# Kernel optimization log

Hardware: AMD Instinct MI355X
Metric: run time of the kernel (lower is better)

Reference implementation:

```python
import jax, jax.numpy as jnp
import numpy as np

BETA = 0.25
NUM_CODEBOOK = 1024
DIM = 256


def setup_inputs() -> dict:
    key = jax.random.key(0)
    k1, k2 = jax.random.split(key)
    z = jax.random.normal(k1, (32, DIM, 32, 32), dtype=jnp.float32)
    # nn.init.uniform_(weight, -1/num_codebook, 1/num_codebook)
    bound = 1.0 / NUM_CODEBOOK
    codebook = jax.random.uniform(k2, (NUM_CODEBOOK, DIM), dtype=jnp.float32,
                                  minval=-bound, maxval=bound)
    return {"z": z, "codebook": codebook}


def reference(z, codebook):
    B, C, H, W = z.shape
    # NCHW -> NHWC -> [B*H*W, C]
    z_flat = jnp.transpose(z, (0, 2, 3, 1)).reshape(-1, C)
    # squared euclidean distances to each code: [B*H*W, K]
    dist = (jnp.sum(z_flat * z_flat, axis=1, keepdims=True)
            + jnp.sum(codebook * codebook, axis=1)
            - 2.0 * jnp.matmul(z_flat, codebook.T))
    idx = jnp.argmin(dist, axis=-1)                      # [B*H*W]
    z_q = codebook[idx].reshape(B, H, W, C)              # gather
    z_q = jnp.transpose(z_q, (0, 3, 1, 2))               # back to NCHW
    commit_loss = (jnp.mean((jax.lax.stop_gradient(z_q) - z) ** 2)
                   + BETA * jnp.mean((z_q - jax.lax.stop_gradient(z)) ** 2))
    # straight-through estimator
    z_q_st = z + jax.lax.stop_gradient(z_q - z)
    return z_q_st, commit_loss
```

## Files before the change

### kernel.cpp

```cpp
#include <hip/hip_runtime.h>
#include <hip/hip_bf16.h>
#include <hip/hip_fp8.h>
#include <stdint.h>


#define WS_CN    0
#define WS_CB    4096
#define WS_PENC  266240
#define WS_PART2 790528
#define WS_PART  791040

typedef float f32x4 __attribute__((ext_vector_type(4)));
typedef long  i64;
typedef long  l64x2 __attribute__((ext_vector_type(2)));

template <bool HI>
static __device__ __forceinline__ unsigned pk2(float a, float b, unsigned old) {
#if __has_builtin(__builtin_amdgcn_cvt_pk_fp8_f32)
    return (unsigned)__builtin_amdgcn_cvt_pk_fp8_f32(a, b, (int)old, HI);
#else
    __hip_fp8_e4m3 qa(a), qb(b);
    unsigned w = (unsigned)qa.__x | ((unsigned)qb.__x << 8);
    return HI ? ((old & 0x0000FFFFu) | (w << 16)) : ((old & 0xFFFF0000u) | w);
#endif
}

__global__ __launch_bounds__(64) void k0_prep(const float* __restrict__ cb,
                                              float* __restrict__ cn256,
                                              unsigned char* __restrict__ cbf8) {
    const int code = blockIdx.x;
    const int l = threadIdx.x;
    const float4 v = ((const float4*)cb)[code * 64 + l];
    float nrm = v.x * v.x + v.y * v.y + v.z * v.z + v.w * v.w;
    #pragma unroll
    for (int off = 1; off < 64; off <<= 1) nrm += __shfl_xor(nrm, off);
    if (l == 0) cn256[code] = 256.f * nrm;
    unsigned u = pk2<false>(-512.f * v.x, -512.f * v.y, 0u);
    u = pk2<true>(-512.f * v.z, -512.f * v.w, u);
    const int q = code >> 8, chunk = (code >> 4) & 15, r16 = code & 15;
    const int ks = l >> 3, kp = l >> 4, g4 = (l >> 1) & 3;
    const int lane = g4 * 16 + r16;
    const int byteoff = q * 65536 + ((chunk * 4 + kp) * 64 + lane) * 16
                      + (ks & 1) * 8 + (l & 1) * 4;
    *(unsigned*)(cbf8 + byteoff) = u;
}

__global__ __launch_bounds__(512) void k1_main(const float* __restrict__ z,
                                               const unsigned char* __restrict__ cbf8,
                                               const float* __restrict__ cn256,
                                               float* __restrict__ penc,
                                               float* __restrict__ part2) {
    __shared__ __align__(16) unsigned char lds[65536];
    const int t = threadIdx.x, w = t >> 6, l = t & 63;
    const int col = l & 15, g4 = l >> 4, gc4 = g4 * 4;
    const int b = blockIdx.x, q = b >> 7, grp = b & 127;
    const int img = grp >> 2, hw0 = (grp & 3) << 8;

    {
        const unsigned char* src = cbf8 + q * 65536;
        #pragma unroll
        for (int i = 0; i < 8; ++i) {
            const int off = i * 8192 + w * 1024;
            __builtin_amdgcn_global_load_lds(
                (const __attribute__((address_space(1))) unsigned*)(src + off + l * 16),
                (__attribute__((address_space(3))) unsigned*)(lds + off), 16, 0, 0);
        }
    }

    const float* zp = z + img * 262144 + hw0 + w * 32;
    float z2 = 0.f;
    i64 zf[2][8];
    #pragma unroll
    for (int pf = 0; pf < 2; ++pf) {
        const int p = pf * 16 + col;
        #pragma unroll
        for (int ks = 0; ks < 8; ++ks) {
            const float* s0 = zp + (ks * 32 + g4 * 8) * 1024 + p;
            float v0 = s0[0], v1 = s0[1024], v2 = s0[2048], v3 = s0[3072];
            float v4 = s0[4096], v5 = s0[5120], v6 = s0[6144], v7 = s0[7168];
            z2 += v0*v0 + v1*v1 + v2*v2 + v3*v3 + v4*v4 + v5*v5 + v6*v6 + v7*v7;
            unsigned lo = pk2<false>(v0, v1, 0u); lo = pk2<true>(v2, v3, lo);
            unsigned hi = pk2<false>(v4, v5, 0u); hi = pk2<true>(v6, v7, hi);
            zf[pf][ks] = (i64)(((unsigned long)hi << 32) | (unsigned long)lo);
        }
    }
    __syncthreads();

    float menc0 = __builtin_bit_cast(float, 0x7F7FFC00u);
    float menc1 = __builtin_bit_cast(float, 0x7F7FFC00u);

    i64 A0[8], A1[8];
#define LDA(DST, c) do {                                                         \
    _Pragma("unroll") for (int kp = 0; kp < 4; ++kp) {                           \
        l64x2 u = *(const l64x2*)(lds + (((c) * 4 + kp) * 64 + l) * 16);         \
        DST[2 * kp] = u.x; DST[2 * kp + 1] = u.y;                                \
    }                                                                            \
} while (0)
#define BODY(CUR, NXT, c) do {                                                   \
    if ((c) + 1 < 16) LDA(NXT, (c) + 1);                                         \
    f32x4 a0 = {0.f,0.f,0.f,0.f}, a1 = {0.f,0.f,0.f,0.f};                        \
    _Pragma("unroll") for (int ks = 0; ks < 8; ++ks) {                           \
        a0 = __builtin_amdgcn_mfma_f32_16x16x32_fp8_fp8(CUR[ks], zf[0][ks], a0, 0, 0, 0); \
        a1 = __builtin_amdgcn_mfma_f32_16x16x32_fp8_fp8(CUR[ks], zf[1][ks], a1, 0, 0, 0); \
    }                                                                            \
    {                                                                            \
        const f32x4 cn = *(const f32x4*)(cn256 + q * 256 + (c) * 16 + gc4);      \
        _Pragma("unroll") for (int r = 0; r < 4; ++r) {                          \
            const unsigned code0 = (unsigned)(q * 256 + (c) * 16 + gc4 + r);     \
            float s; unsigned e;                                                 \
            s = a0[r] + cn[r];                                                   \
            e = (__builtin_bit_cast(unsigned, s) & 0xFFFFFC00u) | code0;         \
            menc0 = fminf(menc0, __builtin_bit_cast(float, e));                  \
            s = a1[r] + cn[r];                                                   \
            e = (__builtin_bit_cast(unsigned, s) & 0xFFFFFC00u) | code0;         \
            menc1 = fminf(menc1, __builtin_bit_cast(float, e));                  \
        }                                                                        \
    }                                                                            \
} while (0)

    LDA(A0, 0);
    #pragma unroll 1
    for (int c2 = 0; c2 < 16; c2 += 2) {
        BODY(A0, A1, c2);
        BODY(A1, A0, c2 + 1);
    }
#undef BODY
#undef LDA

    menc0 = fminf(menc0, __shfl_xor(menc0, 16));
    menc0 = fminf(menc0, __shfl_xor(menc0, 32));
    menc1 = fminf(menc1, __shfl_xor(menc1, 16));
    menc1 = fminf(menc1, __shfl_xor(menc1, 32));
    const int posbase = img * 1024 + hw0 + w * 32;
    if (l < 16) {
        penc[q * 32768 + posbase + l]      = menc0;
        penc[q * 32768 + posbase + 16 + l] = menc1;
    }

    #pragma unroll
    for (int off = 1; off < 64; off <<= 1) z2 += __shfl_xor(z2, off);
    __syncthreads();
    float* red = (float*)lds;
    if (l == 0) red[w] = z2;
    __syncthreads();
    if (t == 0 && q == 0) {
        float s = 0.f;
        #pragma unroll
        for (int i = 0; i < 8; ++i) s += red[i];
        part2[grp] = s;
    }
}

__global__ __launch_bounds__(256) void k2_out(const float* __restrict__ cbf,
                                              const float* __restrict__ penc,
                                              float* __restrict__ out,
                                              float* __restrict__ part) {
    __shared__ __align__(16) float zqbuf[32 * 260];
    __shared__ unsigned idxl[64];
    const int t = threadIdx.x, b = blockIdx.x;
    const int pos0 = b * 64, img = pos0 >> 10, hw0 = pos0 & 1023;

    if (t < 64) {
        const int pos = pos0 + t;
        const float e = fminf(fminf(penc[pos], penc[32768 + pos]),
                              fminf(penc[65536 + pos], penc[98304 + pos]));
        const unsigned eu = __builtin_bit_cast(unsigned, e);
        idxl[t] = eu & 0x3FFu;
        float myS = __builtin_bit_cast(float, eu & 0xFFFFFC00u);
        #pragma unroll
        for (int off = 1; off < 64; off <<= 1) myS += __shfl_xor(myS, off);
        if (t == 0) part[b] = myS * (1.f / 256.f);
    }

    const float4* cb4 = (const float4*)cbf;
    for (int h = 0; h < 2; ++h) {
        __syncthreads();
        #pragma unroll
        for (int i = 0; i < 8; ++i) {
            const int flat = i * 256 + t;
            const int p = flat >> 6;
            const int qq = flat & 63;
            const unsigned code = idxl[h * 32 + p];
            *(float4*)&zqbuf[p * 260 + qq * 4] = cb4[code * 64 + qq];
        }
        __syncthreads();
        const int p = t & 31, c0 = t >> 5;
        float* ob = out + img * 262144 + hw0 + h * 32 + p;
        #pragma unroll
        for (int cc = 0; cc < 32; ++cc) {
            const int ch = c0 + cc * 8;
            ob[ch * 1024] = zqbuf[p * 260 + ch];
        }
    }
}

__global__ __launch_bounds__(256) void k3_red(const float* __restrict__ part2,
                                              const float* __restrict__ part,
                                              float* __restrict__ out) {
    __shared__ float red[256];
    const int t = threadIdx.x;
    float v = part[t] + part[t + 256];
    if (t < 128) v += part2[t];
    red[t] = v;
    __syncthreads();
    #pragma unroll
    for (int off = 128; off > 0; off >>= 1) {
        if (t < off) red[t] += red[t + off];
        __syncthreads();
    }
    if (t == 0) out[8388608] = 1.25f * red[0] / 8388608.f;
}

extern "C" void kernel_launch(void* const* d_in, const int* in_sizes, int n_in,
                              void* d_out, int out_size, void* d_ws, size_t ws_size,
                              hipStream_t stream) {
    const float* z  = (const float*)d_in[0];
    const float* cb = (const float*)d_in[1];
    float* out = (float*)d_out;
    unsigned char* ws = (unsigned char*)d_ws;
    float* cn256 = (float*)(ws + WS_CN);
    unsigned char* cbf8 = ws + WS_CB;
    float* penc  = (float*)(ws + WS_PENC);
    float* part2 = (float*)(ws + WS_PART2);
    float* part  = (float*)(ws + WS_PART);

    hipLaunchKernelGGL(k0_prep, dim3(1024), dim3(64), 0, stream, cb, cn256, cbf8);
    hipLaunchKernelGGL(k1_main, dim3(512), dim3(512), 0, stream, z, cbf8, cn256, penc, part2);
    hipLaunchKernelGGL(k2_out,  dim3(512), dim3(256), 0, stream, cb, penc, out, part);
    hipLaunchKernelGGL(k3_red,  dim3(1), dim3(256), 0, stream, part2, part, out);
}
```

Before: 45.37 us.

## Fuse codebook prep into main kernel and final reduction into output kernel

```diff
diff --git a/kernel.cpp b/kernel.cpp
--- a/kernel.cpp
+++ b/kernel.cpp
@@ -4,11 +4,10 @@
 #include <stdint.h>
 
 
-#define WS_CN    0
-#define WS_CB    4096
-#define WS_PENC  266240
-#define WS_PART2 790528
-#define WS_PART  791040
+#define WS_PENC  0
+#define WS_PART2 524288
+#define WS_PART  524800
+#define WS_CTR   526848
 
 typedef float f32x4 __attribute__((ext_vector_type(4)));
 typedef long  i64;
@@ -25,45 +24,37 @@
 #endif
 }
 
-__global__ __launch_bounds__(64) void k0_prep(const float* __restrict__ cb,
-                                              float* __restrict__ cn256,
-                                              unsigned char* __restrict__ cbf8) {
-    const int code = blockIdx.x;
-    const int l = threadIdx.x;
-    const float4 v = ((const float4*)cb)[code * 64 + l];
-    float nrm = v.x * v.x + v.y * v.y + v.z * v.z + v.w * v.w;
-    #pragma unroll
-    for (int off = 1; off < 64; off <<= 1) nrm += __shfl_xor(nrm, off);
-    if (l == 0) cn256[code] = 256.f * nrm;
-    unsigned u = pk2<false>(-512.f * v.x, -512.f * v.y, 0u);
-    u = pk2<true>(-512.f * v.z, -512.f * v.w, u);
-    const int q = code >> 8, chunk = (code >> 4) & 15, r16 = code & 15;
-    const int ks = l >> 3, kp = l >> 4, g4 = (l >> 1) & 3;
-    const int lane = g4 * 16 + r16;
-    const int byteoff = q * 65536 + ((chunk * 4 + kp) * 64 + lane) * 16
-                      + (ks & 1) * 8 + (l & 1) * 4;
-    *(unsigned*)(cbf8 + byteoff) = u;
-}
-
 __global__ __launch_bounds__(512) void k1_main(const float* __restrict__ z,
-                                               const unsigned char* __restrict__ cbf8,
-                                               const float* __restrict__ cn256,
+                                               const float* __restrict__ cb,
                                                float* __restrict__ penc,
-                                               float* __restrict__ part2) {
+                                               float* __restrict__ part2,
+                                               unsigned* __restrict__ ctr) {
     __shared__ __align__(16) unsigned char lds[65536];
+    __shared__ float cn_lds[256];
+    __shared__ float redz[8];
     const int t = threadIdx.x, w = t >> 6, l = t & 63;
     const int col = l & 15, g4 = l >> 4, gc4 = g4 * 4;
     const int b = blockIdx.x, q = b >> 7, grp = b & 127;
     const int img = grp >> 2, hw0 = (grp & 3) << 8;
 
+    if (b == 0 && t == 0) *ctr = 0u;
+
     {
-        const unsigned char* src = cbf8 + q * 65536;
-        #pragma unroll
-        for (int i = 0; i < 8; ++i) {
-            const int off = i * 8192 + w * 1024;
-            __builtin_amdgcn_global_load_lds(
-                (const __attribute__((address_space(1))) unsigned*)(src + off + l * 16),
-                (__attribute__((address_space(3))) unsigned*)(lds + off), 16, 0, 0);
+        const int kp = l >> 4, ksb = (l >> 3) & 1, g4w = (l >> 1) & 3, lb = l & 1;
+        const float4* cbq = (const float4*)cb + q * 256 * 64;
+        for (int round = 0; round < 32; ++round) {
+            const int code_local = round * 8 + w;
+            const float4 v = cbq[code_local * 64 + l];
+            float nrm = v.x * v.x + v.y * v.y + v.z * v.z + v.w * v.w;
+            #pragma unroll
+            for (int off = 1; off < 64; off <<= 1) nrm += __shfl_xor(nrm, off);
+            if (l == 0) cn_lds[code_local] = 256.f * nrm;
+            unsigned u = pk2<false>(-512.f * v.x, -512.f * v.y, 0u);
+            u = pk2<true>(-512.f * v.z, -512.f * v.w, u);
+            const int chunk = code_local >> 4, r16 = code_local & 15;
+            const int byteoff = ((chunk * 4 + kp) * 64 + g4w * 16 + r16) * 16
+                              + ksb * 8 + lb * 4;
+            *(unsigned*)(lds + byteoff) = u;
         }
     }
 
@@ -91,9 +82,9 @@
 
     i64 A0[8], A1[8];
 #define LDA(DST, c) do {                                                         \
-    _Pragma("unroll") for (int kp = 0; kp < 4; ++kp) {                           \
-        l64x2 u = *(const l64x2*)(lds + (((c) * 4 + kp) * 64 + l) * 16);         \
-        DST[2 * kp] = u.x; DST[2 * kp + 1] = u.y;                                \
+    _Pragma("unroll") for (int kp2 = 0; kp2 < 4; ++kp2) {                        \
+        l64x2 u = *(const l64x2*)(lds + (((c) * 4 + kp2) * 64 + l) * 16);        \
+        DST[2 * kp2] = u.x; DST[2 * kp2 + 1] = u.y;                              \
     }                                                                            \
 } while (0)
 #define BODY(CUR, NXT, c) do {                                                   \
@@ -104,7 +95,7 @@
         a1 = __builtin_amdgcn_mfma_f32_16x16x32_fp8_fp8(CUR[ks], zf[1][ks], a1, 0, 0, 0); \
     }                                                                            \
     {                                                                            \
-        const f32x4 cn = *(const f32x4*)(cn256 + q * 256 + (c) * 16 + gc4);      \
+        const f32x4 cn = *(const f32x4*)(cn_lds + (c) * 16 + gc4);               \
         _Pragma("unroll") for (int r = 0; r < 4; ++r) {                          \
             const unsigned code0 = (unsigned)(q * 256 + (c) * 16 + gc4 + r);     \
             float s; unsigned e;                                                 \
@@ -139,14 +130,12 @@
 
     #pragma unroll
     for (int off = 1; off < 64; off <<= 1) z2 += __shfl_xor(z2, off);
-    __syncthreads();
-    float* red = (float*)lds;
-    if (l == 0) red[w] = z2;
+    if (l == 0) redz[w] = z2;
     __syncthreads();
     if (t == 0 && q == 0) {
         float s = 0.f;
         #pragma unroll
-        for (int i = 0; i < 8; ++i) s += red[i];
+        for (int i = 0; i < 8; ++i) s += redz[i];
         part2[grp] = s;
     }
 }
@@ -154,9 +143,13 @@
 __global__ __launch_bounds__(256) void k2_out(const float* __restrict__ cbf,
                                               const float* __restrict__ penc,
                                               float* __restrict__ out,
-                                              float* __restrict__ part) {
+                                              float* __restrict__ part,
+                                              const float* __restrict__ part2,
+                                              unsigned* __restrict__ ctr) {
     __shared__ __align__(16) float zqbuf[32 * 260];
     __shared__ unsigned idxl[64];
+    __shared__ float red2[256];
+    __shared__ unsigned lastflag;
     const int t = threadIdx.x, b = blockIdx.x;
     const int pos0 = b * 64, img = pos0 >> 10, hw0 = pos0 & 1023;
 
@@ -192,23 +185,25 @@
             ob[ch * 1024] = zqbuf[p * 260 + ch];
         }
     }
-}
-
-__global__ __launch_bounds__(256) void k3_red(const float* __restrict__ part2,
-                                              const float* __restrict__ part,
-                                              float* __restrict__ out) {
-    __shared__ float red[256];
-    const int t = threadIdx.x;
-    float v = part[t] + part[t + 256];
-    if (t < 128) v += part2[t];
-    red[t] = v;
+
+    if (t == 0) {
+        __threadfence();
+        lastflag = (atomicAdd(ctr, 1u) == 511u) ? 1u : 0u;
+    }
     __syncthreads();
-    #pragma unroll
-    for (int off = 128; off > 0; off >>= 1) {
-        if (t < off) red[t] += red[t + off];
+    if (lastflag) {
+        __threadfence();
+        float v = part[t] + part[t + 256];
+        if (t < 128) v += part2[t];
+        red2[t] = v;
         __syncthreads();
-    }
-    if (t == 0) out[8388608] = 1.25f * red[0] / 8388608.f;
+        #pragma unroll
+        for (int off = 128; off > 0; off >>= 1) {
+            if (t < off) red2[t] += red2[t + off];
+            __syncthreads();
+        }
+        if (t == 0) out[8388608] = 1.25f * red2[0] / 8388608.f;
+    }
 }
 
 extern "C" void kernel_launch(void* const* d_in, const int* in_sizes, int n_in,
@@ -218,14 +213,11 @@
     const float* cb = (const float*)d_in[1];
     float* out = (float*)d_out;
     unsigned char* ws = (unsigned char*)d_ws;
-    float* cn256 = (float*)(ws + WS_CN);
-    unsigned char* cbf8 = ws + WS_CB;
     float* penc  = (float*)(ws + WS_PENC);
     float* part2 = (float*)(ws + WS_PART2);
     float* part  = (float*)(ws + WS_PART);
-
-    hipLaunchKernelGGL(k0_prep, dim3(1024), dim3(64), 0, stream, cb, cn256, cbf8);
-    hipLaunchKernelGGL(k1_main, dim3(512), dim3(512), 0, stream, z, cbf8, cn256, penc, part2);
-    hipLaunchKernelGGL(k2_out,  dim3(512), dim3(256), 0, stream, cb, penc, out, part);
-    hipLaunchKernelGGL(k3_red,  dim3(1), dim3(256), 0, stream, part2, part, out);
-}
+    unsigned* ctr = (unsigned*)(ws + WS_CTR);
+
+    hipLaunchKernelGGL(k1_main, dim3(512), dim3(512), 0, stream, z, cb, penc, part2, ctr);
+    hipLaunchKernelGGL(k2_out,  dim3(512), dim3(256), 0, stream, cb, penc, out, part, part2, ctr);
+}
```

Measured after the change: 82.31 us. 81.4% more time.

## Switch distance GEMM to 32x32x16 FP8 MFMA and fuse final reduction via atomic counter

Applied to the files above, without the earlier changes.

```diff
diff --git a/kernel.cpp b/kernel.cpp
--- a/kernel.cpp
+++ b/kernel.cpp
@@ -9,8 +9,10 @@
 #define WS_PENC  266240
 #define WS_PART2 790528
 #define WS_PART  791040
-
-typedef float f32x4 __attribute__((ext_vector_type(4)));
+#define WS_CTR   793088
+
+typedef float f32x4  __attribute__((ext_vector_type(4)));
+typedef float f32x16 __attribute__((ext_vector_type(16)));
 typedef long  i64;
 typedef long  l64x2 __attribute__((ext_vector_type(2)));
 
@@ -27,9 +29,11 @@
 
 __global__ __launch_bounds__(64) void k0_prep(const float* __restrict__ cb,
                                               float* __restrict__ cn256,
-                                              unsigned char* __restrict__ cbf8) {
+                                              unsigned char* __restrict__ cbf8,
+                                              unsigned* __restrict__ ctr) {
     const int code = blockIdx.x;
     const int l = threadIdx.x;
+    if (code == 0 && l == 0) *ctr = 0u;
     const float4 v = ((const float4*)cb)[code * 64 + l];
     float nrm = v.x * v.x + v.y * v.y + v.z * v.z + v.w * v.w;
     #pragma unroll
@@ -37,11 +41,13 @@
     if (l == 0) cn256[code] = 256.f * nrm;
     unsigned u = pk2<false>(-512.f * v.x, -512.f * v.y, 0u);
     u = pk2<true>(-512.f * v.z, -512.f * v.w, u);
-    const int q = code >> 8, chunk = (code >> 4) & 15, r16 = code & 15;
-    const int ks = l >> 3, kp = l >> 4, g4 = (l >> 1) & 3;
-    const int lane = g4 * 16 + r16;
-    const int byteoff = q * 65536 + ((chunk * 4 + kp) * 64 + lane) * 16
-                      + (ks & 1) * 8 + (l & 1) * 4;
+    const int q = code >> 8, cl_ = code & 255;
+    const int g = cl_ >> 5, r32 = cl_ & 31;
+    const int m = l >> 3;
+    const int sel8 = (l >> 2) & 1;
+    const int h = (l >> 1) & 1;
+    const int byteoff = q * 65536 + ((g * 8 + m) * 64 + h * 32 + r32) * 16
+                      + sel8 * 8 + (l & 1) * 4;
     *(unsigned*)(cbf8 + byteoff) = u;
 }
 
@@ -51,10 +57,13 @@
                                                float* __restrict__ penc,
                                                float* __restrict__ part2) {
     __shared__ __align__(16) unsigned char lds[65536];
+    __shared__ __align__(16) float cnl[256];
+    __shared__ float redz[8];
     const int t = threadIdx.x, w = t >> 6, l = t & 63;
-    const int col = l & 15, g4 = l >> 4, gc4 = g4 * 4;
+    const int h = l >> 5, h4 = h * 4, p32 = l & 31;
     const int b = blockIdx.x, q = b >> 7, grp = b & 127;
     const int img = grp >> 2, hw0 = (grp & 3) << 8;
+    const unsigned qbase = (unsigned)(q * 256);
 
     {
         const unsigned char* src = cbf8 + q * 65536;
@@ -65,88 +74,74 @@
                 (const __attribute__((address_space(1))) unsigned*)(src + off + l * 16),
                 (__attribute__((address_space(3))) unsigned*)(lds + off), 16, 0, 0);
         }
-    }
-
-    const float* zp = z + img * 262144 + hw0 + w * 32;
+        if (w == 0) {
+            const unsigned char* csrc = (const unsigned char*)(cn256 + q * 256);
+            __builtin_amdgcn_global_load_lds(
+                (const __attribute__((address_space(1))) unsigned*)(csrc + l * 16),
+                (__attribute__((address_space(3))) unsigned*)((unsigned char*)cnl), 16, 0, 0);
+        }
+    }
+
+    const float* zp = z + img * 262144 + hw0 + w * 32 + p32;
     float z2 = 0.f;
-    i64 zf[2][8];
-    #pragma unroll
-    for (int pf = 0; pf < 2; ++pf) {
-        const int p = pf * 16 + col;
-        #pragma unroll
-        for (int ks = 0; ks < 8; ++ks) {
-            const float* s0 = zp + (ks * 32 + g4 * 8) * 1024 + p;
-            float v0 = s0[0], v1 = s0[1024], v2 = s0[2048], v3 = s0[3072];
-            float v4 = s0[4096], v5 = s0[5120], v6 = s0[6144], v7 = s0[7168];
-            z2 += v0*v0 + v1*v1 + v2*v2 + v3*v3 + v4*v4 + v5*v5 + v6*v6 + v7*v7;
-            unsigned lo = pk2<false>(v0, v1, 0u); lo = pk2<true>(v2, v3, lo);
-            unsigned hi = pk2<false>(v4, v5, 0u); hi = pk2<true>(v6, v7, hi);
-            zf[pf][ks] = (i64)(((unsigned long)hi << 32) | (unsigned long)lo);
-        }
+    i64 zf[16];
+    #pragma unroll
+    for (int ks = 0; ks < 16; ++ks) {
+        const float* s0 = zp + (ks * 16 + h * 8) * 1024;
+        float v0 = s0[0], v1 = s0[1024], v2 = s0[2048], v3 = s0[3072];
+        float v4 = s0[4096], v5 = s0[5120], v6 = s0[6144], v7 = s0[7168];
+        z2 += v0*v0 + v1*v1 + v2*v2 + v3*v3 + v4*v4 + v5*v5 + v6*v6 + v7*v7;
+        unsigned lo = pk2<false>(v0, v1, 0u); lo = pk2<true>(v2, v3, lo);
+        unsigned hi = pk2<false>(v4, v5, 0u); hi = pk2<true>(v6, v7, hi);
+        zf[ks] = (i64)(((unsigned long)hi << 32) | (unsigned long)lo);
     }
     __syncthreads();
 
-    float menc0 = __builtin_bit_cast(float, 0x7F7FFC00u);
-    float menc1 = __builtin_bit_cast(float, 0x7F7FFC00u);
-
-    i64 A0[8], A1[8];
-#define LDA(DST, c) do {                                                         \
-    _Pragma("unroll") for (int kp = 0; kp < 4; ++kp) {                           \
-        l64x2 u = *(const l64x2*)(lds + (((c) * 4 + kp) * 64 + l) * 16);         \
-        DST[2 * kp] = u.x; DST[2 * kp + 1] = u.y;                                \
-    }                                                                            \
-} while (0)
-#define BODY(CUR, NXT, c) do {                                                   \
-    if ((c) + 1 < 16) LDA(NXT, (c) + 1);                                         \
-    f32x4 a0 = {0.f,0.f,0.f,0.f}, a1 = {0.f,0.f,0.f,0.f};                        \
-    _Pragma("unroll") for (int ks = 0; ks < 8; ++ks) {                           \
-        a0 = __builtin_amdgcn_mfma_f32_16x16x32_fp8_fp8(CUR[ks], zf[0][ks], a0, 0, 0, 0); \
-        a1 = __builtin_amdgcn_mfma_f32_16x16x32_fp8_fp8(CUR[ks], zf[1][ks], a1, 0, 0, 0); \
-    }                                                                            \
-    {                                                                            \
-        const f32x4 cn = *(const f32x4*)(cn256 + q * 256 + (c) * 16 + gc4);      \
-        _Pragma("unroll") for (int r = 0; r < 4; ++r) {                          \
-            const unsigned code0 = (unsigned)(q * 256 + (c) * 16 + gc4 + r);     \
-            float s; unsigned e;                                                 \
-            s = a0[r] + cn[r];                                                   \
-            e = (__builtin_bit_cast(unsigned, s) & 0xFFFFFC00u) | code0;         \
-            menc0 = fminf(menc0, __builtin_bit_cast(float, e));                  \
-            s = a1[r] + cn[r];                                                   \
-            e = (__builtin_bit_cast(unsigned, s) & 0xFFFFFC00u) | code0;         \
-            menc1 = fminf(menc1, __builtin_bit_cast(float, e));                  \
+    float menc = __builtin_bit_cast(float, 0x7F7FFC00u);
+
+#define ENC(g, acc) do {                                                         \
+    _Pragma("unroll") for (int rr = 0; rr < 4; ++rr) {                           \
+        const f32x4 cn = *(const f32x4*)(cnl + (g) * 32 + rr * 8 + h4);          \
+        _Pragma("unroll") for (int r2 = 0; r2 < 4; ++r2) {                       \
+            const float s = (acc)[rr * 4 + r2] + cn[r2];                         \
+            const unsigned e = (__builtin_bit_cast(unsigned, s) & 0xFFFFFC00u)   \
+                             | (qbase + (unsigned)((g) * 32 + rr * 8 + h4 + r2));\
+            menc = fminf(menc, __builtin_bit_cast(float, e));                    \
         }                                                                        \
     }                                                                            \
 } while (0)
 
-    LDA(A0, 0);
-    #pragma unroll 1
-    for (int c2 = 0; c2 < 16; c2 += 2) {
-        BODY(A0, A1, c2);
-        BODY(A1, A0, c2 + 1);
-    }
-#undef BODY
-#undef LDA
-
-    menc0 = fminf(menc0, __shfl_xor(menc0, 16));
-    menc0 = fminf(menc0, __shfl_xor(menc0, 32));
-    menc1 = fminf(menc1, __shfl_xor(menc1, 16));
-    menc1 = fminf(menc1, __shfl_xor(menc1, 32));
-    const int posbase = img * 1024 + hw0 + w * 32;
-    if (l < 16) {
-        penc[q * 32768 + posbase + l]      = menc0;
-        penc[q * 32768 + posbase + 16 + l] = menc1;
-    }
+    #pragma unroll
+    for (int gp = 0; gp < 4; ++gp) {
+        const int ga = gp * 2, gb = ga + 1;
+        f32x16 accA = {0.f,0.f,0.f,0.f,0.f,0.f,0.f,0.f,0.f,0.f,0.f,0.f,0.f,0.f,0.f,0.f};
+        f32x16 accB = {0.f,0.f,0.f,0.f,0.f,0.f,0.f,0.f,0.f,0.f,0.f,0.f,0.f,0.f,0.f,0.f};
+        #pragma unroll
+        for (int m = 0; m < 8; ++m) {
+            const l64x2 ua = *(const l64x2*)(lds + ((ga * 8 + m) * 64 + l) * 16);
+            const l64x2 ub = *(const l64x2*)(lds + ((gb * 8 + m) * 64 + l) * 16);
+            accA = __builtin_amdgcn_mfma_f32_32x32x16_fp8_fp8(ua.x, zf[2 * m],     accA, 0, 0, 0);
+            accB = __builtin_amdgcn_mfma_f32_32x32x16_fp8_fp8(ub.x, zf[2 * m],     accB, 0, 0, 0);
+            accA = __builtin_amdgcn_mfma_f32_32x32x16_fp8_fp8(ua.y, zf[2 * m + 1], accA, 0, 0, 0);
+            accB = __builtin_amdgcn_mfma_f32_32x32x16_fp8_fp8(ub.y, zf[2 * m + 1], accB, 0, 0, 0);
+        }
+        ENC(ga, accA);
+        ENC(gb, accB);
+    }
+#undef ENC
+
+    menc = fminf(menc, __shfl_xor(menc, 32));
+    const int pos = grp * 256 + w * 32 + p32;
+    if (l < 32) penc[q * 32768 + pos] = menc;
 
     #pragma unroll
     for (int off = 1; off < 64; off <<= 1) z2 += __shfl_xor(z2, off);
-    __syncthreads();
-    float* red = (float*)lds;
-    if (l == 0) red[w] = z2;
+    if (l == 0) redz[w] = z2;
     __syncthreads();
     if (t == 0 && q == 0) {
         float s = 0.f;
         #pragma unroll
-        for (int i = 0; i < 8; ++i) s += red[i];
+        for (int i = 0; i < 8; ++i) s += redz[i];
         part2[grp] = s;
     }
 }
@@ -154,9 +149,12 @@
 __global__ __launch_bounds__(256) void k2_out(const float* __restrict__ cbf,
                                               const float* __restrict__ penc,
                                               float* __restrict__ out,
-                                              float* __restrict__ part) {
+                                              float* __restrict__ part,
+                                              const float* __restrict__ part2,
+                                              unsigned* __restrict__ ctr) {
     __shared__ __align__(16) float zqbuf[32 * 260];
     __shared__ unsigned idxl[64];
+    __shared__ unsigned lastflag;
     const int t = threadIdx.x, b = blockIdx.x;
     const int pos0 = b * 64, img = pos0 >> 10, hw0 = pos0 & 1023;
 
@@ -173,42 +171,45 @@
     }
 
     const float4* cb4 = (const float4*)cbf;
-    for (int h = 0; h < 2; ++h) {
+    for (int hh = 0; hh < 2; ++hh) {
         __syncthreads();
         #pragma unroll
         for (int i = 0; i < 8; ++i) {
             const int flat = i * 256 + t;
             const int p = flat >> 6;
             const int qq = flat & 63;
-            const unsigned code = idxl[h * 32 + p];
+            const unsigned code = idxl[hh * 32 + p];
             *(float4*)&zqbuf[p * 260 + qq * 4] = cb4[code * 64 + qq];
         }
         __syncthreads();
         const int p = t & 31, c0 = t >> 5;
-        float* ob = out + img * 262144 + hw0 + h * 32 + p;
+        float* ob = out + img * 262144 + hw0 + hh * 32 + p;
         #pragma unroll
         for (int cc = 0; cc < 32; ++cc) {
             const int ch = c0 + cc * 8;
             ob[ch * 1024] = zqbuf[p * 260 + ch];
         }
     }
-}
-
-__global__ __launch_bounds__(256) void k3_red(const float* __restrict__ part2,
-                                              const float* __restrict__ part,
-                                              float* __restrict__ out) {
-    __shared__ float red[256];
-    const int t = threadIdx.x;
-    float v = part[t] + part[t + 256];
-    if (t < 128) v += part2[t];
-    red[t] = v;
+
+    if (t == 0) {
+        __threadfence();
+        lastflag = (atomicAdd(ctr, 1u) == 511u) ? 1u : 0u;
+    }
     __syncthreads();
-    #pragma unroll
-    for (int off = 128; off > 0; off >>= 1) {
-        if (t < off) red[t] += red[t + off];
+    if (lastflag) {
+        __threadfence();
+        float* red2 = zqbuf;
+        float v = part[t] + part[t + 256];
+        if (t < 128) v += part2[t];
+        red2[t] = v;
         __syncthreads();
-    }
-    if (t == 0) out[8388608] = 1.25f * red[0] / 8388608.f;
+        #pragma unroll
+        for (int off = 128; off > 0; off >>= 1) {
+            if (t < off) red2[t] += red2[t + off];
+            __syncthreads();
+        }
+        if (t == 0) out[8388608] = 1.25f * red2[0] / 8388608.f;
+    }
 }
 
 extern "C" void kernel_launch(void* const* d_in, const int* in_sizes, int n_in,
@@ -223,9 +224,9 @@
     float* penc  = (float*)(ws + WS_PENC);
     float* part2 = (float*)(ws + WS_PART2);
     float* part  = (float*)(ws + WS_PART);
-
-    hipLaunchKernelGGL(k0_prep, dim3(1024), dim3(64), 0, stream, cb, cn256, cbf8);
+    unsigned* ctr = (unsigned*)(ws + WS_CTR);
+
+    hipLaunchKernelGGL(k0_prep, dim3(1024), dim3(64), 0, stream, cb, cn256, cbf8, ctr);
     hipLaunchKernelGGL(k1_main, dim3(512), dim3(512), 0, stream, z, cbf8, cn256, penc, part2);
-    hipLaunchKernelGGL(k2_out,  dim3(512), dim3(256), 0, stream, cb, penc, out, part);
-    hipLaunchKernelGGL(k3_red,  dim3(1), dim3(256), 0, stream, part2, part, out);
-}
+    hipLaunchKernelGGL(k2_out,  dim3(512), dim3(256), 0, stream, cb, penc, out, part, part2, ctr);
+}
```

Result: slower. 59.04 us (+30.1%).
